# Kernel optimization log

Hardware: AMD Instinct MI355X
Metric: run time of the kernel (lower is better)

The kernel has to match this reference:

```python
import jax, jax.numpy as jnp
import numpy as np

H = 16          # num_heads
D = 64          # head_dim = dim // num_heads
ROPE_THETA = 10000.0
NEG = -1e9


def _rope_angles(n, d):
    # matches get_1d_rotary_pos_embed(head_dim, N): freqs_cis = polar(1, t outer (theta^-(2i/d)))
    inv_freq = 1.0 / (ROPE_THETA ** (jnp.arange(0, d, 2, dtype=jnp.float32) / d))  # [d/2]
    ang = jnp.arange(n, dtype=jnp.float32)[:, None] * inv_freq[None, :]            # [n, d/2]
    return jnp.cos(ang), jnp.sin(ang)


def _apply_rope(x, cos, sin):
    # x: [B,H,N,D]; complex rotation on adjacent pairs (use_real=False semantics)
    x0 = x[..., 0::2]
    x1 = x[..., 1::2]
    # broadcast cos/sin [N, D/2] over batch and heads
    r0 = x0 * cos - x1 * sin
    r1 = x0 * sin + x1 * cos
    return jnp.stack([r0, r1], axis=-1).reshape(x.shape)


def setup_inputs() -> dict:
    key = jax.random.key(0)
    ks = jax.random.split(key, 5)
    B, N, C = 4, 2048, 1024
    s_in = 1.0 / np.sqrt(C)
    return {
        "x": jax.random.normal(ks[0], (B, N, C), dtype=jnp.float32),
        "Wqkv_w": jax.random.normal(ks[1], (3 * C, C), dtype=jnp.float32) * s_in,
        "Wqkv_b": jax.random.normal(ks[2], (3 * C,), dtype=jnp.float32) * 0.01,
        "out_w": jax.random.normal(ks[3], (C, C), dtype=jnp.float32) * s_in,
        "out_b": jax.random.normal(ks[4], (C,), dtype=jnp.float32) * 0.01,
    }


def reference(x, Wqkv_w, Wqkv_b, out_w, out_b):
    B, N, C = x.shape
    scale = D ** -0.5
    # fused QKV projection: [B,N,3C] -> [3,B,H,N,D]
    qkv = (jnp.einsum('bnc,oc->bno', x, Wqkv_w) + Wqkv_b)
    qkv = qkv.reshape(B, N, 3, H, D).transpose(2, 0, 3, 1, 4)
    q, k, v = qkv[0], qkv[1], qkv[2]
    # qk_norm=False -> Identity
    cos, sin = _rope_angles(N, D)
    q = _apply_rope(q, cos, sin)
    k = _apply_rope(k, cos, sin)
    attn = jnp.einsum('bhqd,bhkd->bhqk', q * scale, k)      # [B,H,N,N]
    causal = jnp.triu(jnp.ones((N, N), dtype=bool), k=1)
    attn = jnp.where(causal[None, None], NEG, attn)
    attn = jax.nn.softmax(attn, axis=-1)
    o = jnp.einsum('bhqk,bhkd->bhqd', attn, v)              # [B,H,N,D]
    o = o.transpose(0, 2, 1, 3).reshape(B, N, C)
    return jnp.einsum('bnc,oc->bno', o, out_w) + out_b
```

## Files before the change

kernel.cpp:

```cpp
#include <hip/hip_runtime.h>
#include <hip/hip_bf16.h>

#define DEVI __device__ __forceinline__

typedef __attribute__((ext_vector_type(8))) short short8v;
typedef __attribute__((ext_vector_type(4))) float f32x4;
typedef __attribute__((ext_vector_type(2))) unsigned u32x2;

DEVI short f2bf(float f) {
  __hip_bfloat16 h = __float2bfloat16(f);
  return __builtin_bit_cast(short, h);
}
DEVI float bf2f(short s) {
  unsigned u = ((unsigned)(unsigned short)s) << 16;
  return __builtin_bit_cast(float, u);
}
DEVI unsigned packbf(float a, float b) {
  return (unsigned)(unsigned short)f2bf(a) | ((unsigned)(unsigned short)f2bf(b) << 16);
}
DEVI void gload16(const void* g, void* l) {
  __builtin_amdgcn_global_load_lds((const __attribute__((address_space(1))) void*)g,
                                   (__attribute__((address_space(3))) void*)l, 16, 0, 0);
}
#define MFMA16(a, b, c) __builtin_amdgcn_mfma_f32_16x16x32_bf16((a), (b), (c), 0, 0, 0)


__global__ void cvt_all(const float* __restrict__ x, const float* __restrict__ wq,
                        const float* __restrict__ wo, short* __restrict__ xb,
                        short* __restrict__ wqb, short* __restrict__ wob) {
  int i = blockIdx.x * blockDim.x + threadIdx.x;
  const float* in;
  short* out;
  if (i < 2097152) { in = x; out = xb; }
  else if (i < 2097152 + 786432) { in = wq; out = wqb; i -= 2097152; }
  else { in = wo; out = wob; i -= 2097152 + 786432; }
  float4 v = ((const float4*)in)[i];
  short4 o;
  o.x = f2bf(v.x); o.y = f2bf(v.y); o.z = f2bf(v.z); o.w = f2bf(v.w);
  ((short4*)out)[i] = o;
}

__global__ void rope_table(float2* __restrict__ tbl) {
  int i = blockIdx.x * blockDim.x + threadIdx.x;
  int n = i >> 5, f = i & 31;
  float inv = powf(10000.0f, -(float)f * (1.0f / 32.0f));
  float ang = (float)n * inv;
  tbl[i] = make_float2(cosf(ang), sinf(ang));
}

__global__ void rope_k(short* __restrict__ kk, const float2* __restrict__ tbl) {
  int i = blockIdx.x * blockDim.x + threadIdx.x;
  int row = i >> 3, c8 = i & 7;
  int n = row & 2047;
  short* ad = kk + (size_t)row * 64 + c8 * 8;
  short8v vv = *(short8v*)ad;
  short8v ov;
#pragma unroll
  for (int j = 0; j < 4; ++j) {
    float2 cs = tbl[n * 32 + c8 * 4 + j];
    float x0 = bf2f(vv[2 * j]), x1 = bf2f(vv[2 * j + 1]);
    ov[2 * j]     = f2bf(x0 * cs.x - x1 * cs.y);
    ov[2 * j + 1] = f2bf(x0 * cs.y + x1 * cs.x);
  }
  *(short8v*)ad = ov;
}

__global__ __launch_bounds__(512, 2)
void gemm256(const short* __restrict__ A, const short* __restrict__ Bw,
             const float* __restrict__ bias,
             short* __restrict__ q, short* __restrict__ k, short* __restrict__ v,
             int Kdim) {
  __shared__ __attribute__((aligned(16))) short lds[65536];
  const int t = threadIdx.x;
  const int lane = t & 63, w = t >> 6;
  const int wr = w >> 2, wc = w & 3;
  const int g = lane >> 4, r16 = lane & 15;
  const int n0 = blockIdx.x * 256, m0 = blockIdx.y * 256;

  int goffs[4], loffs[4];
#pragma unroll
  for (int p = 0; p < 4; ++p) {
    int c = p * 512 + t;
    int row = c >> 3, u = c & 7;
    goffs[p] = row * Kdim + ((u ^ (row & 7)) * 8);
    loffs[p] = c * 16;
  }
  const short* Abase = A + (size_t)m0 * Kdim;
  const short* Bbase = Bw + (size_t)n0 * Kdim;

  auto STAGE = [&](int s, int k0) {
#pragma unroll
    for (int p = 0; p < 4; ++p) {
      gload16(Abase + k0 + goffs[p], (char*)lds + s * 32768 + loffs[p]);
      gload16(Bbase + k0 + goffs[p], (char*)lds + 65536 + s * 32768 + loffs[p]);
    }
  };

  f32x4 acc[8][4];
#pragma unroll
  for (int i = 0; i < 8; ++i)
#pragma unroll
    for (int j = 0; j < 4; ++j) acc[i][j] = (f32x4){0.f, 0.f, 0.f, 0.f};

  const int nsteps = Kdim >> 6;
  STAGE(0, 0);
  __syncthreads();

  int cur = 0;
  for (int st = 0; st < nsteps; ++st) {
    if (st + 1 < nsteps) STAGE(cur ^ 1, (st + 1) << 6);
    const char* Ab = (const char*)lds + cur * 32768;
    const char* Bb = (const char*)lds + 65536 + cur * 32768;
#pragma unroll
    for (int ks = 0; ks < 2; ++ks) {
      short8v bf[4];
#pragma unroll
      for (int ni = 0; ni < 4; ++ni) {
        int rowb = wc * 64 + ni * 16 + r16;
        bf[ni] = *(const short8v*)(Bb + rowb * 128 + (((ks * 4 + g) ^ (rowb & 7)) << 4));
      }
#pragma unroll
      for (int mi = 0; mi < 8; ++mi) {
        int rowa = wr * 128 + mi * 16 + r16;
        short8v af =
            *(const short8v*)(Ab + rowa * 128 + (((ks * 4 + g) ^ (rowa & 7)) << 4));
#pragma unroll
        for (int ni = 0; ni < 4; ++ni)
          acc[mi][ni] = MFMA16(af, bf[ni], acc[mi][ni]);
      }
    }
    __syncthreads();
    cur ^= 1;
  }

  const int b = m0 >> 11, nb = m0 & 2047;
  if (n0 < 2048) {
#pragma unroll
    for (int ni = 0; ni < 4; ++ni) {
      int col = n0 + wc * 64 + ni * 16 + r16;
      float bv = bias[col];
      int s = col >> 10, h = (col & 1023) >> 6, d = col & 63;
      short* dst = (s == 0) ? q : k;
#pragma unroll
      for (int mi = 0; mi < 8; ++mi) {
        int mrow = m0 + wr * 128 + mi * 16 + g * 4;
#pragma unroll
        for (int r = 0; r < 4; ++r) {
          int n = (mrow + r) & 2047;
          dst[(((size_t)(b * 16 + h)) * 2048 + n) * 64 + d] = f2bf(acc[mi][ni][r] + bv);
        }
      }
    }
  } else {
    short* Cs = lds;
    const int hdrb = (n0 - 2048) >> 6;
#pragma unroll
    for (int hh = 0; hh < 4; ++hh) {
      if (wc == hh) {
#pragma unroll
        for (int ni = 0; ni < 4; ++ni) {
          float bv = bias[n0 + hh * 64 + ni * 16 + r16];
#pragma unroll
          for (int mi = 0; mi < 8; ++mi) {
            u32x2 pk;
            pk[0] = packbf(acc[mi][ni][0] + bv, acc[mi][ni][1] + bv);
            pk[1] = packbf(acc[mi][ni][2] + bv, acc[mi][ni][3] + bv);
            *(u32x2*)&Cs[(ni * 16 + r16) * 264 + wr * 128 + mi * 16 + g * 4] = pk;
          }
        }
      }
      __syncthreads();
      short* vdst = v + ((size_t)(b * 16 + hdrb + hh)) * 64 * 2048;
#pragma unroll
      for (int j = 0; j < 4; ++j) {
        int chunk = j * 512 + t;
        int d = chunk >> 5, c = chunk & 31;
        short8v val = *(const short8v*)&Cs[d * 264 + c * 8];
        *(short8v*)(vdst + (size_t)d * 2048 + nb + c * 8) = val;
      }
      __syncthreads();
    }
  }
}

__global__ __launch_bounds__(256)
void gemm_f32(const short* __restrict__ A, const short* __restrict__ Bw,
              const float* __restrict__ bias, float* __restrict__ fout,
              int Ndim, int Kdim) {
  __shared__ __attribute__((aligned(16))) short As[3][128 * 32];
  __shared__ __attribute__((aligned(16))) short Bs[3][128 * 32];
  const int t = threadIdx.x;
  const int lane = t & 63, w = t >> 6;
  const int wr = w >> 1, wc = w & 1;
  const int g = lane >> 4, r16 = lane & 15;
  const int m0 = blockIdx.y * 128, n0 = blockIdx.x * 128;

  int goffs[2], loffs[2];
#pragma unroll
  for (int p = 0; p < 2; ++p) {
    int c = p * 256 + t;
    int row = c >> 2, u = c & 3;
    goffs[p] = row * Kdim + ((u ^ ((row >> 1) & 3)) * 8);
    loffs[p] = c * 16;
  }
  const short* Abase = A + (size_t)m0 * Kdim;
  const short* Bbase = Bw + (size_t)n0 * Kdim;

  auto STAGE = [&](int s, int k0) {
#pragma unroll
    for (int p = 0; p < 2; ++p) {
      gload16(Abase + k0 + goffs[p], (char*)&As[s][0] + loffs[p]);
      gload16(Bbase + k0 + goffs[p], (char*)&Bs[s][0] + loffs[p]);
    }
  };

  f32x4 acc[4][4];
#pragma unroll
  for (int i = 0; i < 4; ++i)
#pragma unroll
    for (int j = 0; j < 4; ++j) acc[i][j] = (f32x4){0.f, 0.f, 0.f, 0.f};

  const int nsteps = Kdim >> 5;
  STAGE(0, 0);
  STAGE(1, 32);
  asm volatile("s_waitcnt vmcnt(4)" ::: "memory");
  __builtin_amdgcn_s_barrier();
  asm volatile("" ::: "memory");

  int cur = 0, pre = 2;
  const int rsw = (r16 >> 1) & 3;
  for (int st = 0; st < nsteps; ++st) {
    if (st + 2 < nsteps) STAGE(pre, (st + 2) << 5);
    short8v af[4], bf[4];
#pragma unroll
    for (int mi = 0; mi < 4; ++mi)
      af[mi] = *(const short8v*)&As[cur][(wr * 64 + mi * 16 + r16) * 32 +
                                         ((g ^ rsw) * 8)];
#pragma unroll
    for (int ni = 0; ni < 4; ++ni)
      bf[ni] = *(const short8v*)&Bs[cur][(wc * 64 + ni * 16 + r16) * 32 +
                                         ((g ^ rsw) * 8)];
#pragma unroll
    for (int mi = 0; mi < 4; ++mi)
#pragma unroll
      for (int ni = 0; ni < 4; ++ni)
        acc[mi][ni] = MFMA16(af[mi], bf[ni], acc[mi][ni]);
    if (st + 2 < nsteps) asm volatile("s_waitcnt vmcnt(4)" ::: "memory");
    else                 asm volatile("s_waitcnt vmcnt(0)" ::: "memory");
    __builtin_amdgcn_s_barrier();
    asm volatile("" ::: "memory");
    cur = (cur == 2) ? 0 : cur + 1;
    pre = (pre == 2) ? 0 : pre + 1;
  }

#pragma unroll
  for (int ni = 0; ni < 4; ++ni) {
    int col = n0 + wc * 64 + ni * 16 + r16;
    float bv = bias[col];
#pragma unroll
    for (int mi = 0; mi < 4; ++mi) {
      int mrow = m0 + wr * 64 + mi * 16 + g * 4;
#pragma unroll
      for (int r = 0; r < 4; ++r)
        fout[(size_t)(mrow + r) * Ndim + col] = acc[mi][ni][r] + bv;
    }
  }
}

__global__ __launch_bounds__(256)
void fattn(const short* __restrict__ q, const short* __restrict__ k,
           const short* __restrict__ vT, const float2* __restrict__ tbl,
           short* __restrict__ o) {
  const int bx = blockIdx.x;
  const int qt = 15 - (bx >> 6);
  const int bh = bx & 63;
  const int b = bh >> 4, h = bh & 15;
  const int t = threadIdx.x, lane = t & 63, w = t >> 6;
  const int g = lane >> 4, r16 = lane & 15;

  __shared__ __attribute__((aligned(16))) short Ks[2][64 * 64];
  __shared__ __attribute__((aligned(16))) short Vt[2][64 * 64];
  __shared__ __attribute__((aligned(16))) short Ps[4][2][16 * 72];

  const short* qb = q + (size_t)bh * 2048 * 64;
  const short* kb = k + (size_t)bh * 2048 * 64;
  const short* vb = vT + (size_t)bh * 2048 * 64;

  int koffs[2], voffs[2], loffs[2];
#pragma unroll
  for (int p = 0; p < 2; ++p) {
    int c = p * 256 + t;
    int row = c >> 3, u = c & 7;
    int x8 = (u ^ (row & 7)) * 8;
    koffs[p] = row * 64 + x8;
    voffs[p] = row * 2048 + x8;
    loffs[p] = c * 16;
  }
  auto STAGE = [&](int s, int kt) {
#pragma unroll
    for (int p = 0; p < 2; ++p) {
      gload16(kb + (size_t)kt * 4096 + koffs[p], (char*)&Ks[s][0] + loffs[p]);
      gload16(vb + kt * 64 + voffs[p], (char*)&Vt[s][0] + loffs[p]);
    }
  };

  const int q0 = qt * 128 + w * 32;

  const float sc = 0.125f * 1.44269504088896f;
  short8v aq[2][2];
#pragma unroll
  for (int qi = 0; qi < 2; ++qi) {
    const int n = q0 + qi * 16 + r16;
#pragma unroll
    for (int dk = 0; dk < 2; ++dk) {
      short8v raw = *(const short8v*)(qb + (size_t)n * 64 + dk * 32 + g * 8);
      short8v rq;
#pragma unroll
      for (int j = 0; j < 4; ++j) {
        float2 cs = tbl[n * 32 + dk * 16 + g * 4 + j];
        float x0 = bf2f(raw[2 * j]), x1 = bf2f(raw[2 * j + 1]);
        rq[2 * j]     = f2bf((x0 * cs.x - x1 * cs.y) * sc);
        rq[2 * j + 1] = f2bf((x0 * cs.y + x1 * cs.x) * sc);
      }
      aq[qi][dk] = rq;
    }
  }

  const short one_bf = 0x3F80;
  const short8v ones = {one_bf, one_bf, one_bf, one_bf, one_bf, one_bf, one_bf, one_bf};
  const float M = 24.0f;

  f32x4 oacc[2][4], lacc[2];
#pragma unroll
  for (int qi = 0; qi < 2; ++qi) {
#pragma unroll
    for (int dc = 0; dc < 4; ++dc) oacc[qi][dc] = (f32x4){0.f, 0.f, 0.f, 0.f};
    lacc[qi] = (f32x4){0.f, 0.f, 0.f, 0.f};
  }

  const int ktmax = 2 * qt + 1;

  STAGE(0, 0);
  __syncthreads();

  for (int kt = 0; kt <= ktmax; ++kt) {
    const int cur = kt & 1;
    if (kt < ktmax) STAGE(cur ^ 1, kt + 1);

    const bool act0 = (kt * 64 <= q0 + 15);
    const bool act1 = (kt * 64 <= q0 + 31);

    f32x4 s[2][4];
#pragma unroll
    for (int qi = 0; qi < 2; ++qi)
#pragma unroll
      for (int kc = 0; kc < 4; ++kc) s[qi][kc] = (f32x4){0.f, 0.f, 0.f, 0.f};

    if (act1) {
      __builtin_amdgcn_s_setprio(1);
#pragma unroll
      for (int kc = 0; kc < 4; ++kc) {
        int key = kc * 16 + r16;
        const char* rb = (const char*)&Ks[cur][0] + key * 128;
        short8v kf0 = *(const short8v*)(rb + (((g) ^ (key & 7)) << 4));
        short8v kf1 = *(const short8v*)(rb + (((4 + g) ^ (key & 7)) << 4));
        if (act0) {
          s[0][kc] = MFMA16(kf0, aq[0][0], s[0][kc]);
          s[0][kc] = MFMA16(kf1, aq[0][1], s[0][kc]);
        }
        s[1][kc] = MFMA16(kf0, aq[1][0], s[1][kc]);
        s[1][kc] = MFMA16(kf1, aq[1][1], s[1][kc]);
      }
      __builtin_amdgcn_s_setprio(0);

#pragma unroll
      for (int qi = 0; qi < 2; ++qi) {
        if (qi == 0 && !act0) continue;
        const int qrow = q0 + qi * 16 + r16;
        const bool needmask = (kt * 64 + 63 > q0 + qi * 16);
        if (needmask) {
#pragma unroll
          for (int kc = 0; kc < 4; ++kc)
#pragma unroll
            for (int r = 0; r < 4; ++r)
              if (kt * 64 + kc * 16 + g * 4 + r > qrow) s[qi][kc][r] = -1e30f;
        }
        unsigned pk[4][2];
#pragma unroll
        for (int kc = 0; kc < 4; ++kc) {
          float p0 = __builtin_amdgcn_exp2f(s[qi][kc][0] - M);
          float p1 = __builtin_amdgcn_exp2f(s[qi][kc][1] - M);
          float p2 = __builtin_amdgcn_exp2f(s[qi][kc][2] - M);
          float p3 = __builtin_amdgcn_exp2f(s[qi][kc][3] - M);
          pk[kc][0] = packbf(p0, p1);
          pk[kc][1] = packbf(p2, p3);
        }
#pragma unroll
        for (int kc = 0; kc < 4; ++kc)
          *(u32x2*)((char*)&Ps[w][qi][0] + r16 * 144 + kc * 32 + g * 8) =
              (u32x2){pk[kc][0], pk[kc][1]};
      }

      asm volatile("" ::: "memory");

      short8v pa[2][2];
#pragma unroll
      for (int qi = 0; qi < 2; ++qi) {
        if (qi == 0 && !act0) continue;
#pragma unroll
        for (int kk = 0; kk < 2; ++kk)
          pa[qi][kk] =
              *(const short8v*)((char*)&Ps[w][qi][0] + r16 * 144 + kk * 64 + g * 16);
      }
      __builtin_amdgcn_s_setprio(1);
      if (act0) {
        lacc[0] = MFMA16(pa[0][0], ones, lacc[0]);
        lacc[0] = MFMA16(pa[0][1], ones, lacc[0]);
      }
      lacc[1] = MFMA16(pa[1][0], ones, lacc[1]);
      lacc[1] = MFMA16(pa[1][1], ones, lacc[1]);
#pragma unroll
      for (int dc = 0; dc < 4; ++dc) {
        int d = dc * 16 + r16;
        const char* vr = (const char*)&Vt[cur][0] + d * 128;
#pragma unroll
        for (int kk = 0; kk < 2; ++kk) {
          short8v bv = *(const short8v*)(vr + (((kk * 4 + g) ^ (d & 7)) << 4));
          if (act0) oacc[0][dc] = MFMA16(pa[0][kk], bv, oacc[0][dc]);
          oacc[1][dc] = MFMA16(pa[1][kk], bv, oacc[1][dc]);
        }
      }
      __builtin_amdgcn_s_setprio(0);
    }
    __syncthreads();
  }

#pragma unroll
  for (int qi = 0; qi < 2; ++qi) {
#pragma unroll
    for (int r = 0; r < 4; ++r) {
      float ilr = 1.f / lacc[qi][r];
      int qg = q0 + qi * 16 + g * 4 + r;
      short* orow = o + ((size_t)(b * 2048 + qg)) * 1024 + h * 64;
#pragma unroll
      for (int dc = 0; dc < 4; ++dc)
        orow[dc * 16 + r16] = f2bf(oacc[qi][dc][r] * ilr);
    }
  }
}

extern "C" void kernel_launch(void* const* d_in, const int* in_sizes, int n_in,
                              void* d_out, int out_size, void* d_ws, size_t ws_size,
                              hipStream_t stream) {
  const float* x    = (const float*)d_in[0];
  const float* Wqkv = (const float*)d_in[1];
  const float* bqkv = (const float*)d_in[2];
  const float* Wout = (const float*)d_in[3];
  const float* bout = (const float*)d_in[4];

  char* p = (char*)d_ws;
  short* xb = (short*)p;    p += (size_t)8192 * 1024 * 2;
  short* wqkvb = (short*)p; p += (size_t)3072 * 1024 * 2;
  short* woutb = (short*)p; p += (size_t)1024 * 1024 * 2;
  short* qbf = (short*)p;   p += (size_t)64 * 2048 * 64 * 2;
  short* kbf = (short*)p;   p += (size_t)64 * 2048 * 64 * 2;
  short* vbf = (short*)p;   p += (size_t)64 * 2048 * 64 * 2;
  float2* tbl = (float2*)p; p += (size_t)2048 * 32 * 8;

  cvt_all<<<12288, 256, 0, stream>>>(x, Wqkv, Wout, xb, wqkvb, woutb);
  rope_table<<<256, 256, 0, stream>>>(tbl);

  gemm256<<<dim3(12, 32), 512, 0, stream>>>(xb, wqkvb, bqkv, qbf, kbf, vbf, 1024);
  rope_k<<<4096, 256, 0, stream>>>(kbf, tbl);
  fattn<<<dim3(1024), 256, 0, stream>>>(qbf, kbf, vbf, tbl, xb);
  gemm_f32<<<dim3(8, 64), 256, 0, stream>>>(xb, woutb, bout, (float*)d_out, 1024, 1024);
}
```

Measured before the change: 189.1 us.

## Halve QKV GEMM K-step to shrink LDS; use 256-row query tiles in attention

The QKV GEMM now stages 32-wide K slices instead of 64, with a new XOR swizzle for the 64-byte rows. This halves LDS use to 64KB so that two 512-thread blocks can share a CU, at the cost of twice as many barrier-separated steps. The attention kernel moves to 512 threads, each block covering 256 query rows. This doubles reuse of every staged K/V tile and halves the grid, with a new ordering of query tiles to balance the causal workload. The risk is fewer blocks in flight and more per-step overhead in the GEMM.

```diff
diff --git a/kernel.cpp b/kernel.cpp
--- a/kernel.cpp
+++ b/kernel.cpp
@@ -70,19 +70,19 @@
              const float* __restrict__ bias,
              short* __restrict__ q, short* __restrict__ k, short* __restrict__ v,
              int Kdim) {
-  __shared__ __attribute__((aligned(16))) short lds[65536];
+  __shared__ __attribute__((aligned(16))) short lds[32768];
   const int t = threadIdx.x;
   const int lane = t & 63, w = t >> 6;
   const int wr = w >> 2, wc = w & 3;
   const int g = lane >> 4, r16 = lane & 15;
   const int n0 = blockIdx.x * 256, m0 = blockIdx.y * 256;
 
-  int goffs[4], loffs[4];
-#pragma unroll
-  for (int p = 0; p < 4; ++p) {
+  int goffs[2], loffs[2];
+#pragma unroll
+  for (int p = 0; p < 2; ++p) {
     int c = p * 512 + t;
-    int row = c >> 3, u = c & 7;
-    goffs[p] = row * Kdim + ((u ^ (row & 7)) * 8);
+    int row = c >> 2, u = c & 3;
+    goffs[p] = row * Kdim + ((u ^ ((row >> 1) & 3)) * 8);
     loffs[p] = c * 16;
   }
   const short* Abase = A + (size_t)m0 * Kdim;
@@ -90,9 +90,9 @@
 
   auto STAGE = [&](int s, int k0) {
 #pragma unroll
-    for (int p = 0; p < 4; ++p) {
+    for (int p = 0; p < 2; ++p) {
       gload16(Abase + k0 + goffs[p], (char*)lds + s * 32768 + loffs[p]);
-      gload16(Bbase + k0 + goffs[p], (char*)lds + 65536 + s * 32768 + loffs[p]);
+      gload16(Bbase + k0 + goffs[p], (char*)lds + s * 32768 + 16384 + loffs[p]);
     }
   };
 
@@ -102,32 +102,29 @@
 #pragma unroll
     for (int j = 0; j < 4; ++j) acc[i][j] = (f32x4){0.f, 0.f, 0.f, 0.f};
 
-  const int nsteps = Kdim >> 6;
+  const int nsteps = Kdim >> 5;
   STAGE(0, 0);
   __syncthreads();
 
+  const int rsw = (r16 >> 1) & 3;
   int cur = 0;
   for (int st = 0; st < nsteps; ++st) {
-    if (st + 1 < nsteps) STAGE(cur ^ 1, (st + 1) << 6);
+    if (st + 1 < nsteps) STAGE(cur ^ 1, (st + 1) << 5);
     const char* Ab = (const char*)lds + cur * 32768;
-    const char* Bb = (const char*)lds + 65536 + cur * 32768;
-#pragma unroll
-    for (int ks = 0; ks < 2; ++ks) {
-      short8v bf[4];
-#pragma unroll
-      for (int ni = 0; ni < 4; ++ni) {
-        int rowb = wc * 64 + ni * 16 + r16;
-        bf[ni] = *(const short8v*)(Bb + rowb * 128 + (((ks * 4 + g) ^ (rowb & 7)) << 4));
-      }
-#pragma unroll
-      for (int mi = 0; mi < 8; ++mi) {
-        int rowa = wr * 128 + mi * 16 + r16;
-        short8v af =
-            *(const short8v*)(Ab + rowa * 128 + (((ks * 4 + g) ^ (rowa & 7)) << 4));
-#pragma unroll
-        for (int ni = 0; ni < 4; ++ni)
-          acc[mi][ni] = MFMA16(af, bf[ni], acc[mi][ni]);
-      }
+    const char* Bb = Ab + 16384;
+    short8v bf[4];
+#pragma unroll
+    for (int ni = 0; ni < 4; ++ni) {
+      int rowb = wc * 64 + ni * 16 + r16;
+      bf[ni] = *(const short8v*)(Bb + rowb * 64 + ((g ^ rsw) << 4));
+    }
+#pragma unroll
+    for (int mi = 0; mi < 8; ++mi) {
+      int rowa = wr * 128 + mi * 16 + r16;
+      short8v af = *(const short8v*)(Ab + rowa * 64 + ((g ^ rsw) << 4));
+#pragma unroll
+      for (int ni = 0; ni < 4; ++ni)
+        acc[mi][ni] = MFMA16(af, bf[ni], acc[mi][ni]);
     }
     __syncthreads();
     cur ^= 1;
@@ -267,12 +264,13 @@
   }
 }
 
-__global__ __launch_bounds__(256)
+__global__ __launch_bounds__(512)
 void fattn(const short* __restrict__ q, const short* __restrict__ k,
            const short* __restrict__ vT, const float2* __restrict__ tbl,
            short* __restrict__ o) {
   const int bx = blockIdx.x;
-  const int qt = 15 - (bx >> 6);
+  const int idx = bx >> 6;
+  const int qt = (idx < 4) ? (7 - idx) : (idx - 4);
   const int bh = bx & 63;
   const int b = bh >> 4, h = bh & 15;
   const int t = threadIdx.x, lane = t & 63, w = t >> 6;
@@ -280,31 +278,23 @@
 
   __shared__ __attribute__((aligned(16))) short Ks[2][64 * 64];
   __shared__ __attribute__((aligned(16))) short Vt[2][64 * 64];
-  __shared__ __attribute__((aligned(16))) short Ps[4][2][16 * 72];
+  __shared__ __attribute__((aligned(16))) short Ps[8][2][16 * 72];
 
   const short* qb = q + (size_t)bh * 2048 * 64;
   const short* kb = k + (size_t)bh * 2048 * 64;
   const short* vb = vT + (size_t)bh * 2048 * 64;
 
-  int koffs[2], voffs[2], loffs[2];
-#pragma unroll
-  for (int p = 0; p < 2; ++p) {
-    int c = p * 256 + t;
-    int row = c >> 3, u = c & 7;
-    int x8 = (u ^ (row & 7)) * 8;
-    koffs[p] = row * 64 + x8;
-    voffs[p] = row * 2048 + x8;
-    loffs[p] = c * 16;
-  }
+  const int srow = t >> 3, su = t & 7;
+  const int sx8 = (su ^ (srow & 7)) * 8;
+  const int koff = srow * 64 + sx8;
+  const int voff = srow * 2048 + sx8;
+  const int loff = t * 16;
   auto STAGE = [&](int s, int kt) {
-#pragma unroll
-    for (int p = 0; p < 2; ++p) {
-      gload16(kb + (size_t)kt * 4096 + koffs[p], (char*)&Ks[s][0] + loffs[p]);
-      gload16(vb + kt * 64 + voffs[p], (char*)&Vt[s][0] + loffs[p]);
-    }
+    gload16(kb + (size_t)kt * 4096 + koff, (char*)&Ks[s][0] + loff);
+    gload16(vb + kt * 64 + voff, (char*)&Vt[s][0] + loff);
   };
 
-  const int q0 = qt * 128 + w * 32;
+  const int q0 = qt * 256 + w * 32;
 
   const float sc = 0.125f * 1.44269504088896f;
   short8v aq[2][2];
@@ -338,7 +328,7 @@
     lacc[qi] = (f32x4){0.f, 0.f, 0.f, 0.f};
   }
 
-  const int ktmax = 2 * qt + 1;
+  const int ktmax = 4 * qt + 3;
 
   STAGE(0, 0);
   __syncthreads();
@@ -472,6 +462,6 @@
 
   gemm256<<<dim3(12, 32), 512, 0, stream>>>(xb, wqkvb, bqkv, qbf, kbf, vbf, 1024);
   rope_k<<<4096, 256, 0, stream>>>(kbf, tbl);
-  fattn<<<dim3(1024), 256, 0, stream>>>(qbf, kbf, vbf, tbl, xb);
+  fattn<<<dim3(512), 512, 0, stream>>>(qbf, kbf, vbf, tbl, xb);
   gemm_f32<<<dim3(8, 64), 256, 0, stream>>>(xb, woutb, bout, (float*)d_out, 1024, 1024);
 }
```

After: 188.2 us. Within noise of the previous version (-0.5%).
